# Kernel tuning notes

Measured on AMD Instinct MI355X. Metric: run time of the kernel, lower is better.

The kernel has to match this reference:

```python
import jax, jax.numpy as jnp
import numpy as np

N, NFEAT, NHID, NCLASS, NHEADS = 3072, 128, 64, 64, 8
ALPHA = 0.2  # LeakyReLU negative slope
NEG = -9e15  # masking value from pyGAT


def gat_layer(h, mask, W, a):
    # h: [N, Fin]; mask: [N, N] bool; W: [H, Fin, Fout]; a: [H, 2*Fout]
    fout = W.shape[-1]
    Wh = jnp.einsum('ni,hio->hno', h, W)            # [H, N, Fout]
    e_src = jnp.einsum('hno,ho->hn', Wh, a[:, :fout])
    e_dst = jnp.einsum('hno,ho->hn', Wh, a[:, fout:])
    e = jax.nn.leaky_relu(e_src[:, :, None] + e_dst[:, None, :], ALPHA)  # [H,N,N]
    e = jnp.where(mask[None], e, NEG)
    att = jax.nn.softmax(e, axis=-1)                 # dropout is identity in eval
    out = jnp.einsum('hnm,hmo->hno', att, Wh)        # [H, N, Fout]
    out = jax.nn.elu(out)                            # concat=True -> elu
    # concat heads along feature dim: [N, H*Fout]
    return out.transpose(1, 0, 2).reshape(h.shape[0], -1)


def setup_inputs() -> dict:
    key = jax.random.key(0)
    ks = jax.random.split(key, 10)
    x = jax.random.normal(ks[0], (N, NFEAT), dtype=jnp.float32)
    adj = (jax.random.uniform(ks[1], (N, N)) < 0.01).astype(jnp.float32)
    adj = jnp.maximum(adj, jnp.eye(N, dtype=jnp.float32))
    hid = NHID * NHEADS
    dims = [(NFEAT, NHID), (hid, NHID), (hid, NHID), (hid, NCLASS)]
    params = {}
    for i, (fin, fout) in enumerate(dims):
        kw, ka = jax.random.split(ks[2 + i])
        params[f'W{i+1}'] = jax.random.normal(kw, (NHEADS, fin, fout), dtype=jnp.float32) * (1.0 / np.sqrt(fin))
        params[f'a{i+1}'] = jax.random.normal(ka, (NHEADS, 2 * fout), dtype=jnp.float32) * 0.1
    return {'x': x, 'adj': adj, **params}


def reference(x, adj, W1, a1, W2, a2, W3, a3, W4, a4):
    mask = adj > 0
    h = gat_layer(x, mask, W1, a1)
    h = gat_layer(h, mask, W2, a2)
    h = gat_layer(h, mask, W3, a3)
    h = gat_layer(h, mask, W4, a4)
    return h  # [N, NHEADS*NCLASS]
```

## Files before the change

kernel.cpp:

```cpp
#include <hip/hip_runtime.h>
#include <math.h>

#define NN 3072
#define NH 8
#define FO 64
#define FCAT 512
#define MAXDEG 128
#define ALPHA 0.2f

typedef __attribute__((ext_vector_type(8))) short bf16x8;
typedef __attribute__((ext_vector_type(4))) float f32x4;

static __device__ __forceinline__ unsigned short f2bf(float v) {
    union { float f; unsigned u; } x; x.f = v;
    unsigned r = x.u + 0x7fffu + ((x.u >> 16) & 1u);
    return (unsigned short)(r >> 16);
}
static __device__ __forceinline__ float bf2f(unsigned short b) {
    union { unsigned u; float f; } x; x.u = ((unsigned)b) << 16;
    return x.f;
}

__global__ __launch_bounds__(256) void prelude_k(const float* __restrict__ x,
                                                 const float* __restrict__ adj,
                                                 const float* __restrict__ W1,
                                                 const float* __restrict__ W2,
                                                 const float* __restrict__ W3,
                                                 const float* __restrict__ W4,
                                                 unsigned short* __restrict__ Ah,
                                                 unsigned short* __restrict__ Al,
                                                 unsigned short* __restrict__ Wth,
                                                 unsigned short* __restrict__ Wtl,
                                                 int* __restrict__ deg,
                                                 int* __restrict__ nbr) {
    __shared__ float t[64][65];
    const int b = blockIdx.x, tid = threadIdx.x;

    if (b < 256) {
        int base = b * 1536 + tid;
        #pragma unroll
        for (int i = 0; i < 6; ++i) {
            int idx = base + i * 256;
            float v = x[idx];
            unsigned short hb = f2bf(v);
            Ah[idx] = hb;
            Al[idx] = f2bf(v - bf2f(hb));
        }
        if (b < 208) {
            const float* W; int K; int local; size_t obase;
            if (b < 16)       { W = W1; K = 128; local = b;       obase = 0; }
            else if (b < 80)  { W = W2; K = 512; local = b - 16;  obase = 65536; }
            else if (b < 144) { W = W3; K = 512; local = b - 80;  obase = 327680; }
            else              { W = W4; K = 512; local = b - 144; obase = 589824; }
            int nkt = K >> 6;
            int h = local / nkt, kt = local - h * nkt;
            int k0 = kt * 64;
            for (int idx = tid; idx < 4096; idx += 256) {
                int r = idx >> 6, c = idx & 63;
                t[r][c] = W[(size_t)h * K * FO + (size_t)(k0 + r) * FO + c];
            }
            __syncthreads();
            for (int idx = tid; idx < 4096; idx += 256) {
                int o = idx >> 6, kk = idx & 63;
                float v = t[kk][o];
                unsigned short hb = f2bf(v);
                size_t dst = obase + (size_t)(h * FO + o) * K + k0 + kk;
                Wth[dst] = hb;
                Wtl[dst] = f2bf(v - bf2f(hb));
            }
        }
    } else {
        int row = (b - 256) * 4 + (tid >> 6);
        int lane = tid & 63;
        const float* arow = adj + (size_t)row * NN;
        int count = 0;
        for (int base = 0; base < NN; base += 64) {
            float v = arow[base + lane];
            unsigned long long m = __ballot(v > 0.0f);
            if (v > 0.0f) {
                int pos = count + __popcll(m & ((1ull << lane) - 1ull));
                if (pos < MAXDEG) nbr[(size_t)row * MAXDEG + pos] = base + lane;
            }
            count += __popcll(m);
        }
        if (lane == 0) deg[row] = count < MAXDEG ? count : MAXDEG;
    }
}

__global__ __launch_bounds__(256, 3) void gemm_ee_k(const unsigned short* __restrict__ Ah,
                                                    const unsigned short* __restrict__ Al,
                                                    const unsigned short* __restrict__ Bh,
                                                    const unsigned short* __restrict__ Bl,
                                                    const float* __restrict__ a,
                                                    float* __restrict__ C,
                                                    float* __restrict__ esrc,
                                                    float* __restrict__ edst, int K) {
    __shared__ __align__(16) unsigned char smem[30720];
    typedef float CsT[68];
    unsigned short* As_ = (unsigned short*)smem;
    unsigned short* Bs_ = (unsigned short*)(smem + 10240);
    CsT* Cs = reinterpret_cast<CsT*>(smem);

    const int tid = threadIdx.x;
    const int h = blockIdx.x;
    const int r0 = blockIdx.y * 32;
    const int lane = tid & 63;
    const int wid = tid >> 6;
    const int wr = wid >> 1, wc = wid & 1;
    const int lr = lane & 15, lg = lane >> 4;

    const unsigned short* Bhh = Bh + (size_t)h * FO * K;
    const unsigned short* Bll = Bl + (size_t)h * FO * K;

    const int row0 = tid >> 3, cq0 = tid & 7;
    const int off0 = row0 * 80 + ((cq0 ^ (row0 & 7)) * 8);
    const size_t gA0 = (size_t)(r0 + row0) * K + cq0 * 8;
    const size_t gB0 = (size_t)row0 * K + cq0 * 8;
    const size_t gB1 = gB0 + (size_t)32 * K;

    bf16x8 rah, ral, rb0h, rb0l, rb1h, rb1l;

    auto loadg = [&](int k0) {
        rah = *(const bf16x8*)(Ah + gA0 + k0);
        ral = *(const bf16x8*)(Al + gA0 + k0);
        rb0h = *(const bf16x8*)(Bhh + gB0 + k0);
        rb0l = *(const bf16x8*)(Bll + gB0 + k0);
        rb1h = *(const bf16x8*)(Bhh + gB1 + k0);
        rb1l = *(const bf16x8*)(Bll + gB1 + k0);
    };
    auto store_lds = [&]() {
        *(bf16x8*)&As_[off0] = rah;
        *(bf16x8*)&As_[2560 + off0] = ral;
        *(bf16x8*)&Bs_[off0] = rb0h;
        *(bf16x8*)&Bs_[5120 + off0] = rb0l;
        *(bf16x8*)&Bs_[off0 + 2560] = rb1h;
        *(bf16x8*)&Bs_[5120 + off0 + 2560] = rb1l;
    };

    f32x4 acc[2];
    acc[0] = (f32x4){0.f, 0.f, 0.f, 0.f};
    acc[1] = (f32x4){0.f, 0.f, 0.f, 0.f};

    auto mfma_phase = [&]() {
        #pragma unroll
        for (int ks = 0; ks < 2; ++ks) {
            int cq = ks * 4 + lg;
            int arow = wr * 16 + lr;
            int offa = arow * 80 + ((cq ^ (arow & 7)) * 8);
            bf16x8 ah = *(const bf16x8*)&As_[offa];
            bf16x8 al = *(const bf16x8*)&As_[2560 + offa];
            bf16x8 bh[2], bl[2];
            #pragma unroll
            for (int j = 0; j < 2; ++j) {
                int col = wc * 32 + j * 16 + lr;
                int offb = col * 80 + ((cq ^ (col & 7)) * 8);
                bh[j] = *(const bf16x8*)&Bs_[offb];
                bl[j] = *(const bf16x8*)&Bs_[5120 + offb];
            }
            #pragma unroll
            for (int j = 0; j < 2; ++j) {
                acc[j] = __builtin_amdgcn_mfma_f32_16x16x32_bf16(ah, bh[j], acc[j], 0, 0, 0);
                acc[j] = __builtin_amdgcn_mfma_f32_16x16x32_bf16(ah, bl[j], acc[j], 0, 0, 0);
                acc[j] = __builtin_amdgcn_mfma_f32_16x16x32_bf16(al, bh[j], acc[j], 0, 0, 0);
            }
        }
    };

    loadg(0);
    store_lds();
    __syncthreads();
    for (int k0 = 64; k0 < K; k0 += 64) {
        loadg(k0);
        mfma_phase();
        __syncthreads();
        store_lds();
        __syncthreads();
    }
    mfma_phase();
    __syncthreads();

    #pragma unroll
    for (int j = 0; j < 2; ++j)
        #pragma unroll
        for (int r = 0; r < 4; ++r)
            Cs[wr * 16 + lg * 4 + r][wc * 32 + j * 16 + lr] = acc[j][r];
    __syncthreads();

    #pragma unroll
    for (int it = 0; it < 2; ++it) {
        int idx = tid + it * 256;
        int r = idx >> 4, c4 = idx & 15;
        *(float4*)&C[(size_t)(r0 + r) * FCAT + h * FO + c4 * 4] = *(float4*)&Cs[r][c4 * 4];
    }

    {
        int r = tid >> 3, sub = tid & 7;
        const float* av = a + h * 2 * FO;
        float s = 0.0f, dd = 0.0f;
        #pragma unroll
        for (int k = 0; k < 8; ++k) {
            float v = Cs[r][sub * 8 + k];
            s = fmaf(v, av[sub * 8 + k], s);
            dd = fmaf(v, av[FO + sub * 8 + k], dd);
        }
        s += __shfl_xor(s, 1); s += __shfl_xor(s, 2); s += __shfl_xor(s, 4);
        dd += __shfl_xor(dd, 1); dd += __shfl_xor(dd, 2); dd += __shfl_xor(dd, 4);
        if (sub == 0) {
            esrc[h * NN + r0 + r] = s;
            edst[h * NN + r0 + r] = dd;
        }
    }
}

__global__ __launch_bounds__(256) void attn_agg_k(const float* __restrict__ Wh,
                                                  const float* __restrict__ esrc,
                                                  const float* __restrict__ edst,
                                                  const int* __restrict__ deg,
                                                  const int* __restrict__ nbr,
                                                  float* __restrict__ outp,
                                                  unsigned short* __restrict__ oh,
                                                  unsigned short* __restrict__ ol,
                                                  int write_f32) {
    __shared__ float pbuf[4][MAXDEG];
    __shared__ int jbuf[4][MAXDEG];
    const int ws = threadIdx.x >> 6;
    const int lane = threadIdx.x & 63;
    const int h = blockIdx.x / (NN / 4);
    const int n = (blockIdx.x % (NN / 4)) * 4 + ws;
    const int d = deg[n];
    const int* nb = nbr + (size_t)n * MAXDEG;
    const float es = esrc[h * NN + n];
    const float* ed = edst + h * NN;

    for (int t = lane; t < d; t += 64) {
        int j = nb[t];
        float e = es + ed[j];
        e = (e > 0.0f) ? e : ALPHA * e;
        jbuf[ws][t] = j;
        pbuf[ws][t] = e;
    }
    float lm = -3.0e38f;
    for (int t = lane; t < d; t += 64) lm = fmaxf(lm, pbuf[ws][t]);
    #pragma unroll
    for (int off = 32; off; off >>= 1) lm = fmaxf(lm, __shfl_xor(lm, off));
    float lsum = 0.0f;
    for (int t = lane; t < d; t += 64) {
        float pv = __expf(pbuf[ws][t] - lm);
        pbuf[ws][t] = pv;
        lsum += pv;
    }
    #pragma unroll
    for (int off = 32; off; off >>= 1) lsum += __shfl_xor(lsum, off);

    const float* whb = Wh + h * FO + lane;
    float a0 = 0.f, a1 = 0.f, a2 = 0.f, a3 = 0.f;
    int t = 0;
    for (; t + 3 < d; t += 4) {
        a0 = fmaf(pbuf[ws][t + 0], whb[(size_t)jbuf[ws][t + 0] * FCAT], a0);
        a1 = fmaf(pbuf[ws][t + 1], whb[(size_t)jbuf[ws][t + 1] * FCAT], a1);
        a2 = fmaf(pbuf[ws][t + 2], whb[(size_t)jbuf[ws][t + 2] * FCAT], a2);
        a3 = fmaf(pbuf[ws][t + 3], whb[(size_t)jbuf[ws][t + 3] * FCAT], a3);
    }
    for (; t < d; ++t)
        a0 = fmaf(pbuf[ws][t], whb[(size_t)jbuf[ws][t] * FCAT], a0);
    float acc = (a0 + a1) + (a2 + a3);
    acc /= lsum;
    float r = (acc > 0.0f) ? acc : (__expf(acc) - 1.0f);
    size_t idx = (size_t)n * FCAT + h * FO + lane;
    if (write_f32) {
        outp[idx] = r;
    } else {
        unsigned short hb = f2bf(r);
        oh[idx] = hb;
        ol[idx] = f2bf(r - bf2f(hb));
    }
}

extern "C" void kernel_launch(void* const* d_in, const int* in_sizes, int n_in,
                              void* d_out, int out_size, void* d_ws, size_t ws_size,
                              hipStream_t stream) {
    const float* x   = (const float*)d_in[0];
    const float* adj = (const float*)d_in[1];
    const float* ap[4] = {(const float*)d_in[3], (const float*)d_in[5],
                          (const float*)d_in[7], (const float*)d_in[9]};
    float* out = (float*)d_out;

    char* p = (char*)d_ws;
    int* deg = (int*)p;              p += (size_t)NN * sizeof(int);
    int* nbr = (int*)p;              p += (size_t)NN * MAXDEG * sizeof(int);
    unsigned short* Ah = (unsigned short*)p; p += (size_t)NN * FCAT * 2;
    unsigned short* Al = (unsigned short*)p; p += (size_t)NN * FCAT * 2;
    float* WhF = (float*)p;          p += (size_t)NN * FCAT * sizeof(float);
    unsigned short* Wth = (unsigned short*)p; p += (size_t)851968 * 2;
    unsigned short* Wtl = (unsigned short*)p; p += (size_t)851968 * 2;
    float* esrc = (float*)p;         p += (size_t)NN * NH * sizeof(float);
    float* edst = (float*)p;         p += (size_t)NN * NH * sizeof(float);

    prelude_k<<<1024, 256, 0, stream>>>(x, adj,
                                        (const float*)d_in[2], (const float*)d_in[4],
                                        (const float*)d_in[6], (const float*)d_in[8],
                                        Ah, Al, Wth, Wtl, deg, nbr);

    const size_t woff[4] = {0, 65536, 327680, 589824};
    int K = 128;
    for (int L = 0; L < 4; ++L) {
        dim3 g(NH, NN / 32);
        gemm_ee_k<<<g, 256, 0, stream>>>(Ah, Al, Wth + woff[L], Wtl + woff[L],
                                         ap[L], WhF, esrc, edst, K);
        attn_agg_k<<<NH * (NN / 4), 256, 0, stream>>>(WhF, esrc, edst, deg, nbr,
                                                      out, Ah, Al, L == 3 ? 1 : 0);
        K = FCAT;
    }
}
```

Before: 140.9 us.

## Process four heads per wave in attention aggregation with node-major score layout

Stores the source and destination attention scores node-major (16 floats per node) so one float4 load fetches four heads' destination scores per neighbour. Each wave now handles four heads of one node: it computes four softmaxes and aggregates with float4 gathers of Wh rows, with 16 lanes per head. The grid shrinks fourfold and the outputs are written as vectors. This targets gather traffic and the cost of recomputing neighbour indices once per head, at the price of more per-wave serial softmax work and higher register use.

```diff
diff --git a/kernel.cpp b/kernel.cpp
--- a/kernel.cpp
+++ b/kernel.cpp
@@ -6,6 +6,7 @@
 #define FO 64
 #define FCAT 512
 #define MAXDEG 128
+#define PBPAD 136
 #define ALPHA 0.2f
 
 typedef __attribute__((ext_vector_type(8))) short bf16x8;
@@ -93,8 +94,7 @@
                                                     const unsigned short* __restrict__ Bl,
                                                     const float* __restrict__ a,
                                                     float* __restrict__ C,
-                                                    float* __restrict__ esrc,
-                                                    float* __restrict__ edst, int K) {
+                                                    float* __restrict__ ee, int K) {
     __shared__ __align__(16) unsigned char smem[30720];
     typedef float CsT[68];
     unsigned short* As_ = (unsigned short*)smem;
@@ -206,73 +206,113 @@
         s += __shfl_xor(s, 1); s += __shfl_xor(s, 2); s += __shfl_xor(s, 4);
         dd += __shfl_xor(dd, 1); dd += __shfl_xor(dd, 2); dd += __shfl_xor(dd, 4);
         if (sub == 0) {
-            esrc[h * NN + r0 + r] = s;
-            edst[h * NN + r0 + r] = dd;
+            ee[(size_t)(r0 + r) * 16 + h] = s;
+            ee[(size_t)(r0 + r) * 16 + 8 + h] = dd;
         }
     }
 }
 
 __global__ __launch_bounds__(256) void attn_agg_k(const float* __restrict__ Wh,
-                                                  const float* __restrict__ esrc,
-                                                  const float* __restrict__ edst,
+                                                  const float* __restrict__ ee,
                                                   const int* __restrict__ deg,
                                                   const int* __restrict__ nbr,
                                                   float* __restrict__ outp,
                                                   unsigned short* __restrict__ oh,
                                                   unsigned short* __restrict__ ol,
                                                   int write_f32) {
-    __shared__ float pbuf[4][MAXDEG];
+    __shared__ float pbuf[4][4][PBPAD];
     __shared__ int jbuf[4][MAXDEG];
     const int ws = threadIdx.x >> 6;
     const int lane = threadIdx.x & 63;
-    const int h = blockIdx.x / (NN / 4);
+    const int hg = blockIdx.x / (NN / 4);
     const int n = (blockIdx.x % (NN / 4)) * 4 + ws;
+    const int h0 = hg * 4;
     const int d = deg[n];
     const int* nb = nbr + (size_t)n * MAXDEG;
-    const float es = esrc[h * NN + n];
-    const float* ed = edst + h * NN;
-
+    float (*pb)[PBPAD] = pbuf[ws];
+
+    const float es0 = ee[(size_t)n * 16 + h0];
+    const float es1 = ee[(size_t)n * 16 + h0 + 1];
+    const float es2 = ee[(size_t)n * 16 + h0 + 2];
+    const float es3 = ee[(size_t)n * 16 + h0 + 3];
     for (int t = lane; t < d; t += 64) {
         int j = nb[t];
-        float e = es + ed[j];
-        e = (e > 0.0f) ? e : ALPHA * e;
         jbuf[ws][t] = j;
-        pbuf[ws][t] = e;
-    }
-    float lm = -3.0e38f;
-    for (int t = lane; t < d; t += 64) lm = fmaxf(lm, pbuf[ws][t]);
+        float4 ed4 = *(const float4*)&ee[(size_t)j * 16 + 8 + h0];
+        float e0 = es0 + ed4.x; e0 = (e0 > 0.0f) ? e0 : ALPHA * e0;
+        float e1 = es1 + ed4.y; e1 = (e1 > 0.0f) ? e1 : ALPHA * e1;
+        float e2 = es2 + ed4.z; e2 = (e2 > 0.0f) ? e2 : ALPHA * e2;
+        float e3 = es3 + ed4.w; e3 = (e3 > 0.0f) ? e3 : ALPHA * e3;
+        pb[0][t] = e0; pb[1][t] = e1; pb[2][t] = e2; pb[3][t] = e3;
+    }
+
+    float lsum[4];
     #pragma unroll
-    for (int off = 32; off; off >>= 1) lm = fmaxf(lm, __shfl_xor(lm, off));
-    float lsum = 0.0f;
-    for (int t = lane; t < d; t += 64) {
-        float pv = __expf(pbuf[ws][t] - lm);
-        pbuf[ws][t] = pv;
-        lsum += pv;
-    }
-    #pragma unroll
-    for (int off = 32; off; off >>= 1) lsum += __shfl_xor(lsum, off);
-
-    const float* whb = Wh + h * FO + lane;
-    float a0 = 0.f, a1 = 0.f, a2 = 0.f, a3 = 0.f;
+    for (int hh = 0; hh < 4; ++hh) {
+        float lm = -3.0e38f;
+        for (int t = lane; t < d; t += 64) lm = fmaxf(lm, pb[hh][t]);
+        #pragma unroll
+        for (int off = 32; off; off >>= 1) lm = fmaxf(lm, __shfl_xor(lm, off));
+        float s = 0.0f;
+        for (int t = lane; t < d; t += 64) {
+            float pv = __expf(pb[hh][t] - lm);
+            pb[hh][t] = pv;
+            s += pv;
+        }
+        #pragma unroll
+        for (int off = 32; off; off >>= 1) s += __shfl_xor(s, off);
+        lsum[hh] = s;
+    }
+
+    const int lg = lane >> 4;
+    const float* whb = Wh + hg * 256 + lane * 4;
+    float4 a0 = {0.f,0.f,0.f,0.f}, a1 = a0, a2 = a0, a3 = a0;
     int t = 0;
     for (; t + 3 < d; t += 4) {
-        a0 = fmaf(pbuf[ws][t + 0], whb[(size_t)jbuf[ws][t + 0] * FCAT], a0);
-        a1 = fmaf(pbuf[ws][t + 1], whb[(size_t)jbuf[ws][t + 1] * FCAT], a1);
-        a2 = fmaf(pbuf[ws][t + 2], whb[(size_t)jbuf[ws][t + 2] * FCAT], a2);
-        a3 = fmaf(pbuf[ws][t + 3], whb[(size_t)jbuf[ws][t + 3] * FCAT], a3);
-    }
-    for (; t < d; ++t)
-        a0 = fmaf(pbuf[ws][t], whb[(size_t)jbuf[ws][t] * FCAT], a0);
-    float acc = (a0 + a1) + (a2 + a3);
-    acc /= lsum;
-    float r = (acc > 0.0f) ? acc : (__expf(acc) - 1.0f);
-    size_t idx = (size_t)n * FCAT + h * FO + lane;
+        int j0 = jbuf[ws][t], j1 = jbuf[ws][t+1], j2 = jbuf[ws][t+2], j3 = jbuf[ws][t+3];
+        float p0 = pb[lg][t], p1 = pb[lg][t+1], p2 = pb[lg][t+2], p3 = pb[lg][t+3];
+        float4 v0 = *(const float4*)&whb[(size_t)j0 * FCAT];
+        float4 v1 = *(const float4*)&whb[(size_t)j1 * FCAT];
+        float4 v2 = *(const float4*)&whb[(size_t)j2 * FCAT];
+        float4 v3 = *(const float4*)&whb[(size_t)j3 * FCAT];
+        a0.x = fmaf(p0, v0.x, a0.x); a0.y = fmaf(p0, v0.y, a0.y);
+        a0.z = fmaf(p0, v0.z, a0.z); a0.w = fmaf(p0, v0.w, a0.w);
+        a1.x = fmaf(p1, v1.x, a1.x); a1.y = fmaf(p1, v1.y, a1.y);
+        a1.z = fmaf(p1, v1.z, a1.z); a1.w = fmaf(p1, v1.w, a1.w);
+        a2.x = fmaf(p2, v2.x, a2.x); a2.y = fmaf(p2, v2.y, a2.y);
+        a2.z = fmaf(p2, v2.z, a2.z); a2.w = fmaf(p2, v2.w, a2.w);
+        a3.x = fmaf(p3, v3.x, a3.x); a3.y = fmaf(p3, v3.y, a3.y);
+        a3.z = fmaf(p3, v3.z, a3.z); a3.w = fmaf(p3, v3.w, a3.w);
+    }
+    for (; t < d; ++t) {
+        float p = pb[lg][t];
+        float4 v = *(const float4*)&whb[(size_t)jbuf[ws][t] * FCAT];
+        a0.x = fmaf(p, v.x, a0.x); a0.y = fmaf(p, v.y, a0.y);
+        a0.z = fmaf(p, v.z, a0.z); a0.w = fmaf(p, v.w, a0.w);
+    }
+    float4 acc;
+    acc.x = (a0.x + a1.x) + (a2.x + a3.x);
+    acc.y = (a0.y + a1.y) + (a2.y + a3.y);
+    acc.z = (a0.z + a1.z) + (a2.z + a3.z);
+    acc.w = (a0.w + a1.w) + (a2.w + a3.w);
+    float ls = (lg == 0) ? lsum[0] : (lg == 1) ? lsum[1] : (lg == 2) ? lsum[2] : lsum[3];
+    float inv = 1.0f / ls;
+    acc.x *= inv; acc.y *= inv; acc.z *= inv; acc.w *= inv;
+    acc.x = (acc.x > 0.0f) ? acc.x : (__expf(acc.x) - 1.0f);
+    acc.y = (acc.y > 0.0f) ? acc.y : (__expf(acc.y) - 1.0f);
+    acc.z = (acc.z > 0.0f) ? acc.z : (__expf(acc.z) - 1.0f);
+    acc.w = (acc.w > 0.0f) ? acc.w : (__expf(acc.w) - 1.0f);
+
+    size_t idx = (size_t)n * FCAT + hg * 256 + lane * 4;
     if (write_f32) {
-        outp[idx] = r;
+        *(float4*)&outp[idx] = acc;
     } else {
-        unsigned short hb = f2bf(r);
-        oh[idx] = hb;
-        ol[idx] = f2bf(r - bf2f(hb));
+        unsigned short h0b = f2bf(acc.x), h1b = f2bf(acc.y), h2b = f2bf(acc.z), h3b = f2bf(acc.w);
+        ushort4 hv = {h0b, h1b, h2b, h3b};
+        ushort4 lv = {f2bf(acc.x - bf2f(h0b)), f2bf(acc.y - bf2f(h1b)),
+                      f2bf(acc.z - bf2f(h2b)), f2bf(acc.w - bf2f(h3b))};
+        *(ushort4*)&oh[idx] = hv;
+        *(ushort4*)&ol[idx] = lv;
     }
 }
 
@@ -293,8 +333,7 @@
     float* WhF = (float*)p;          p += (size_t)NN * FCAT * sizeof(float);
     unsigned short* Wth = (unsigned short*)p; p += (size_t)851968 * 2;
     unsigned short* Wtl = (unsigned short*)p; p += (size_t)851968 * 2;
-    float* esrc = (float*)p;         p += (size_t)NN * NH * sizeof(float);
-    float* edst = (float*)p;         p += (size_t)NN * NH * sizeof(float);
+    float* ee = (float*)p;           p += (size_t)NN * 16 * sizeof(float);
 
     prelude_k<<<1024, 256, 0, stream>>>(x, adj,
                                         (const float*)d_in[2], (const float*)d_in[4],
@@ -306,9 +345,9 @@
     for (int L = 0; L < 4; ++L) {
         dim3 g(NH, NN / 32);
         gemm_ee_k<<<g, 256, 0, stream>>>(Ah, Al, Wth + woff[L], Wtl + woff[L],
-                                         ap[L], WhF, esrc, edst, K);
-        attn_agg_k<<<NH * (NN / 4), 256, 0, stream>>>(WhF, esrc, edst, deg, nbr,
-                                                      out, Ah, Al, L == 3 ? 1 : 0);
+                                         ap[L], WhF, ee, K);
+        attn_agg_k<<<2 * (NN / 4), 256, 0, stream>>>(WhF, ee, deg, nbr,
+                                                     out, Ah, Al, L == 3 ? 1 : 0);
         K = FCAT;
     }
 }
```

Measured after the change: 143.5 us. Within noise of the previous version (+1.8%).
